# Kernel optimization log

Measured on AMD Instinct MI355X. Metric: run time of the kernel, lower is better.

Reference implementation:

```python
import jax, jax.numpy as jnp
import numpy as np

B, S, D = 32, 2048, 1024


def setup_inputs() -> dict:
    key = jax.random.key(0)
    k = jax.random.split(key, 7)
    midi_features = jax.random.normal(k[0], (B, S, D), dtype=jnp.float32)
    scale_id = jax.random.randint(k[1], (B,), 0, 3)
    midi_mask = jax.random.randint(k[2], (B, S), 0, 2).astype(jnp.int32)
    # Stacked branch params: index 0=high, 1=mid, 2=low (matches SCALE_TO_ID)
    W = jax.random.normal(k[3], (3, D, D), dtype=jnp.float32) * 0.02  # Linear weight (out,in)
    b = jax.random.normal(k[4], (3, D), dtype=jnp.float32) * 0.02
    scale_embed = jax.random.normal(k[5], (3, D), dtype=jnp.float32) * 0.02
    branch_embed = jax.random.normal(k[6], (3, D), dtype=jnp.float32) * 0.02
    return {"midi_features": midi_features, "scale_id": scale_id, "midi_mask": midi_mask,
            "W": W, "b": b, "scale_embed": scale_embed, "branch_embed": branch_embed}


def reference(midi_features, scale_id, midi_mask, W, b, scale_embed, branch_embed):
    # Per-sample scale routing: gather the branch's Linear weight for each sample
    # (equivalent to the torch fancy-indexing scatter into out[idx]).
    Wb = W[scale_id]               # (B, D, D) torch Linear convention: y = x @ W.T + b
    bb = b[scale_id]               # (B, D)
    out = jax.nn.silu(jnp.einsum('bsd,bed->bse', midi_features, Wb) + bb[:, None, :])
    # Dropout is identity in eval mode.
    out = out + scale_embed[scale_id][:, None, :]       # (B, S, D)

    seq_mask = midi_mask > 0                             # (B, S) bool
    w = seq_mask.astype(out.dtype)[:, :, None]           # (B, S, 1)
    denom = jnp.maximum(w.sum(axis=1), 1e-6)             # (B, 1)
    low_vec = (out * w).sum(axis=1) / denom              # (B, D) masked mean

    high_cond = out + branch_embed[0]                    # (B, S, D)
    mid_cond = out + branch_embed[1]                     # (B, S, D)
    low_cond = low_vec[:, None, :] + branch_embed[2]     # (B, 1, D) weak_low_alignment=True
    return high_cond, mid_cond, low_cond
```

## Files before the change

kernel.cpp:

```cpp
#include <hip/hip_runtime.h>
#include <hip/hip_bf16.h>

#define B_ 32
#define S_ 2048
#define D_ 1024

#define BM 256
#define BN 256
#define BK 64
#define NKT (D_ / BK)

typedef __attribute__((ext_vector_type(8))) short bf16x8;
typedef __attribute__((ext_vector_type(4))) float f32x4;
typedef __attribute__((ext_vector_type(4))) float float4v;

#define AS1 __attribute__((address_space(1)))
#define AS3 __attribute__((address_space(3)))

__device__ __forceinline__ short f2bf(float f) {
    union { float f; unsigned u; } uf;
    uf.f = f;
    unsigned u = uf.u;
    u += 0x7FFFu + ((u >> 16) & 1u);
    return (short)(u >> 16);
}

__global__ __launch_bounds__(256) void cvt_bf16(const float4v* __restrict__ src,
                                                bf16x8* __restrict__ dst, int n8) {
    const int stride = gridDim.x * blockDim.x;
    for (int i = blockIdx.x * blockDim.x + threadIdx.x; i < n8; i += stride) {
        float4v a = src[2 * i], b = src[2 * i + 1];
        bf16x8 v;
#pragma unroll
        for (int j = 0; j < 4; ++j) {
            v[j]     = f2bf(a[j]);
            v[4 + j] = f2bf(b[j]);
        }
        dst[i] = v;
    }
}


#define STAGE_A(nb, h, kt) do {                                               \
    _Pragma("unroll")                                                         \
    for (int j_ = 0; j_ < 2; ++j_) {                                          \
        const int base_ = (h) * 128 + j_ * 64 + wid * 8;                      \
        const int grow_ = j_ * 128 + (h) * 64 + wid * 8 + lrow8;              \
        const __hip_bfloat16* g_ = aBase + (size_t)grow_ * D_ + (kt) * BK + (scb >> 1); \
        __builtin_amdgcn_global_load_lds((const AS1 unsigned int*)g_,         \
            (AS3 unsigned int*)&As[nb][base_ * 64], 16, 0, 0);                \
    } } while (0)

#define STAGE_B(nb, h, kt) do {                                               \
    _Pragma("unroll")                                                         \
    for (int j_ = 0; j_ < 2; ++j_) {                                          \
        const int base_ = (h) * 128 + j_ * 64 + wid * 8;                      \
        const int grow_ = base_ + lrow8;                                      \
        const __hip_bfloat16* g_ = bBase + (size_t)grow_ * D_ + (kt) * BK + (scb >> 1); \
        __builtin_amdgcn_global_load_lds((const AS1 unsigned int*)g_,         \
            (AS3 unsigned int*)&Bs[nb][base_ * 64], 16, 0, 0);                \
    } } while (0)

#define COMPUTE(cur, mh, bh) do {                                             \
    bf16x8 af_[4][2], bv_[2][2];                                              \
    _Pragma("unroll")                                                         \
    for (int mi_ = 0; mi_ < 4; ++mi_) {                                       \
        const int l_ = (mh) * 128 + wm * 64 + mi_ * 16 + fr;                  \
        _Pragma("unroll")                                                     \
        for (int kk_ = 0; kk_ < 2; ++kk_) {                                   \
            const int byt_ = l_ * 128 + ((kk_ * 64 + fg * 16) ^ ((l_ & 7) << 4)); \
            af_[mi_][kk_] = *(const bf16x8*)((const char*)&As[cur][0] + byt_); \
        }                                                                     \
    }                                                                         \
    _Pragma("unroll")                                                         \
    for (int ni_ = 0; ni_ < 2; ++ni_) {                                       \
        const int l_ = (bh) * 128 + wn * 32 + ni_ * 16 + fr;                  \
        _Pragma("unroll")                                                     \
        for (int kk_ = 0; kk_ < 2; ++kk_) {                                   \
            const int byt_ = l_ * 128 + ((kk_ * 64 + fg * 16) ^ ((l_ & 7) << 4)); \
            bv_[ni_][kk_] = *(const bf16x8*)((const char*)&Bs[cur][0] + byt_); \
        }                                                                     \
    }                                                                         \
    __builtin_amdgcn_s_setprio(1);                                            \
    _Pragma("unroll")                                                         \
    for (int mi_ = 0; mi_ < 4; ++mi_)                                         \
        _Pragma("unroll")                                                     \
        for (int ni_ = 0; ni_ < 2; ++ni_)                                     \
            _Pragma("unroll")                                                 \
            for (int kk_ = 0; kk_ < 2; ++kk_)                                 \
                acc[(mh) * 4 + mi_][(bh) * 2 + ni_] =                         \
                    __builtin_amdgcn_mfma_f32_16x16x32_bf16(                  \
                        af_[mi_][kk_], bv_[ni_][kk_],                         \
                        acc[(mh) * 4 + mi_][(bh) * 2 + ni_], 0, 0, 0);        \
    __builtin_amdgcn_s_setprio(0);                                            \
    } while (0)

#define PWAIT() do {                                      \
    asm volatile("s_waitcnt vmcnt(6)" ::: "memory");      \
    asm volatile("s_barrier" ::: "memory"); } while (0)

__global__ __launch_bounds__(512, 2) void fused_gemm_bf16(
    const __hip_bfloat16* __restrict__ aBf,
    const __hip_bfloat16* __restrict__ wBf,
    const int*   __restrict__ scale_id,
    const int*   __restrict__ mask,
    const float* __restrict__ bias,
    const float* __restrict__ scemb,
    const float* __restrict__ bremb,
    float*       __restrict__ out,
    float*       __restrict__ colws)
{
    __shared__ __align__(16) short As[2][BM * BK];
    __shared__ __align__(16) short Bs[2][BM * BK];

    const int tid = threadIdx.x;
    const int lane = tid & 63;
    const int wid = tid >> 6;
    const int wm = wid >> 2;
    const int wn = wid & 3;

    const int NTI = D_ / BN;
    const int MTI = S_ / BM;
    const int NWG = B_ * MTI * NTI;
    const int CPX = NWG / 8;
    int lid = ((int)blockIdx.x % 8) * CPX + ((int)blockIdx.x / 8);
    int nt = lid % NTI;
    int mt = (lid / NTI) % MTI;
    int bb = lid / (NTI * MTI);

    const int sid = scale_id[bb];
    const __hip_bfloat16* aBase = aBf + ((size_t)bb * S_ + (size_t)mt * BM) * D_;
    const __hip_bfloat16* bBase = wBf + ((size_t)sid * D_ + (size_t)nt * BN) * D_;

    const int lrow8 = lane >> 3;
    const int scb = ((lane & 7) * 16) ^ (lrow8 << 4);

    const int fr = lane & 15;
    const int fg = lane >> 4;

    f32x4 acc[8][4];
#pragma unroll
    for (int mi = 0; mi < 8; ++mi)
#pragma unroll
        for (int ni = 0; ni < 4; ++ni)
            acc[mi][ni] = (f32x4){0.f, 0.f, 0.f, 0.f};

    STAGE_B(0, 0, 0); STAGE_A(0, 0, 0); STAGE_B(0, 1, 0); STAGE_A(0, 1, 0);

    for (int kt = 0; kt < NKT; kt += 2) {
        const int k1 = kt + 1;
        const int k1n = (k1 + 1 < NKT) ? k1 + 1 : k1;
        STAGE_B(1, 0, k1);  PWAIT(); COMPUTE(0, 0, 0);
        STAGE_A(1, 0, k1);  PWAIT(); COMPUTE(0, 0, 1);
        STAGE_B(1, 1, k1);  PWAIT(); COMPUTE(0, 1, 0);
        STAGE_A(1, 1, k1);  PWAIT(); COMPUTE(0, 1, 1);
        STAGE_B(0, 0, k1n); PWAIT(); COMPUTE(1, 0, 0);
        STAGE_A(0, 0, k1n); PWAIT(); COMPUTE(1, 0, 1);
        STAGE_B(0, 1, k1n); PWAIT(); COMPUTE(1, 1, 0);
        STAGE_A(0, 1, k1n); PWAIT(); COMPUTE(1, 1, 1);
    }

    __syncthreads();

    const int colb = nt * BN;
    float bv2[2][2], sv2[2][2];
#pragma unroll
    for (int bh = 0; bh < 2; ++bh)
#pragma unroll
        for (int ni = 0; ni < 2; ++ni) {
            const int n = colb + bh * 128 + wn * 32 + ni * 16 + fr;
            bv2[bh][ni] = bias[sid * D_ + n];
            sv2[bh][ni] = scemb[sid * D_ + n];
        }

    float colsum[2][2] = {{0.f, 0.f}, {0.f, 0.f}};
#pragma unroll
    for (int mig = 0; mig < 8; ++mig) {
        const int mrow0 = mt * BM + wm * 128 + mig * 16 + fg * 4;
        float mk[4];
#pragma unroll
        for (int r = 0; r < 4; ++r)
            mk[r] = (mask[(size_t)bb * S_ + mrow0 + r] > 0) ? 1.f : 0.f;
#pragma unroll
        for (int bh = 0; bh < 2; ++bh)
#pragma unroll
            for (int ni = 0; ni < 2; ++ni)
#pragma unroll
                for (int r = 0; r < 4; ++r) {
                    const float v = acc[mig][bh * 2 + ni][r] + bv2[bh][ni];
                    const float o = v / (1.f + __expf(-v)) + sv2[bh][ni];
                    acc[mig][bh * 2 + ni][r] = o;
                    colsum[bh][ni] += mk[r] * o;
                }
    }

#pragma unroll
    for (int bh = 0; bh < 2; ++bh)
#pragma unroll
        for (int ni = 0; ni < 2; ++ni) {
            float s = colsum[bh][ni];
            s += __shfl_xor(s, 16);
            s += __shfl_xor(s, 32);
            if (fg == 0)
                atomicAdd(&colws[(size_t)bb * D_ + (colb + bh * 128 + wn * 32 + ni * 16 + fr)], s);
        }

    float* ldsF = (float*)&As[0][0];
    const float4v b0 = *(const float4v*)&bremb[0 * D_ + colb + lane * 4];
    const float4v b1 = *(const float4v*)&bremb[1 * D_ + colb + lane * 4];
    const size_t MIDOFF = (size_t)B_ * S_ * D_;

#pragma unroll
    for (int mig = 0; mig < 8; ++mig) {
#pragma unroll
        for (int bh = 0; bh < 2; ++bh)
#pragma unroll
            for (int ni = 0; ni < 2; ++ni)
#pragma unroll
                for (int r = 0; r < 4; ++r)
                    ldsF[(wm * 16 + fg * 4 + r) * 260 + bh * 128 + wn * 32 + ni * 16 + fr] =
                        acc[mig][bh * 2 + ni][r];
        __syncthreads();

#pragma unroll
        for (int k = 0; k < 4; ++k) {
            const int lr = wid * 4 + k;
            const int grow = mt * BM + (lr >> 4) * 128 + mig * 16 + (lr & 15);
            const size_t rowbase = ((size_t)bb * S_ + grow) * D_ + colb;
            float4v v = *(const float4v*)&ldsF[lr * 260 + lane * 4];
            __builtin_nontemporal_store(v + b0, (float4v*)&out[rowbase + lane * 4]);
            __builtin_nontemporal_store(v + b1, (float4v*)&out[MIDOFF + rowbase + lane * 4]);
        }
        __syncthreads();
    }
}

#define FBM 128
#define FBN 128
#define FBK 64
#define FNK (D_ / FBK)

__global__ __launch_bounds__(256, 2) void fused_gemm_f32(
    const float* __restrict__ midi,
    const int*   __restrict__ scale_id,
    const int*   __restrict__ mask,
    const float* __restrict__ W,
    const float* __restrict__ bias,
    const float* __restrict__ scemb,
    const float* __restrict__ bremb,
    float*       __restrict__ out,
    float*       __restrict__ ws)
{
    __shared__ __align__(16) short As[FBM * FBK];
    __shared__ __align__(16) short Bs[FBM * FBK];

    const int tid = threadIdx.x;
    const int NTI = D_ / FBN;
    const int MTI = S_ / FBM;
    const int NWG = B_ * MTI * NTI;
    const int CPX = NWG / 8;
    int lid = ((int)blockIdx.x % 8) * CPX + ((int)blockIdx.x / 8);
    int nt = lid % NTI;
    int mt = (lid / NTI) % MTI;
    int bb = lid / (NTI * MTI);

    const int sid = scale_id[bb];
    const float* aBase = midi + ((size_t)bb * S_ + (size_t)mt * FBM) * D_;
    const float* bBase = W + ((size_t)sid * D_ + (size_t)nt * FBN) * D_;

    const int r0 = tid >> 3;
    const int kp = (tid & 7) * 8;

    float4v aL[4], aH[4], bL[4], bH[4];

    auto load_regs = [&](int kt) {
        const int kc = kt * FBK + kp;
#pragma unroll
        for (int i = 0; i < 4; ++i) {
            const float* pa = aBase + (size_t)(r0 + 32 * i) * D_ + kc;
            aL[i] = *(const float4v*)pa;
            aH[i] = *(const float4v*)(pa + 4);
            const float* pb = bBase + (size_t)(r0 + 32 * i) * D_ + kc;
            bL[i] = *(const float4v*)pb;
            bH[i] = *(const float4v*)(pb + 4);
        }
    };

    auto write_lds = [&]() {
#pragma unroll
        for (int i = 0; i < 4; ++i) {
            const int row = r0 + 32 * i;
            const int off = (row * FBK + kp) ^ ((row & 7) << 3);
            bf16x8 va, vb;
#pragma unroll
            for (int j = 0; j < 4; ++j) {
                va[j]     = f2bf(aL[i][j]);
                va[4 + j] = f2bf(aH[i][j]);
                vb[j]     = f2bf(bL[i][j]);
                vb[4 + j] = f2bf(bH[i][j]);
            }
            *(bf16x8*)&As[off] = va;
            *(bf16x8*)&Bs[off] = vb;
        }
    };

    f32x4 acc[4][4];
#pragma unroll
    for (int mi = 0; mi < 4; ++mi)
#pragma unroll
        for (int ni = 0; ni < 4; ++ni)
            acc[mi][ni] = (f32x4){0.f, 0.f, 0.f, 0.f};

    const int lane = tid & 63;
    const int wid = tid >> 6;
    const int wm = wid >> 1, wn = wid & 1;
    const int fr = lane & 15;
    const int fg = lane >> 4;

    load_regs(0);
    write_lds();
    __syncthreads();

    for (int kt = 0; kt < FNK; ++kt) {
        if (kt + 1 < FNK) load_regs(kt + 1);
#pragma unroll
        for (int kk = 0; kk < 2; ++kk) {
            bf16x8 af[4], bfr[4];
#pragma unroll
            for (int mi = 0; mi < 4; ++mi) {
                const int row = wm * 64 + mi * 16 + fr;
                const int off = (row * FBK + kk * 32 + fg * 8) ^ ((row & 7) << 3);
                af[mi] = *(const bf16x8*)&As[off];
            }
#pragma unroll
            for (int ni = 0; ni < 4; ++ni) {
                const int row = wn * 64 + ni * 16 + fr;
                const int off = (row * FBK + kk * 32 + fg * 8) ^ ((row & 7) << 3);
                bfr[ni] = *(const bf16x8*)&Bs[off];
            }
#pragma unroll
            for (int mi = 0; mi < 4; ++mi)
#pragma unroll
                for (int ni = 0; ni < 4; ++ni)
                    acc[mi][ni] = __builtin_amdgcn_mfma_f32_16x16x32_bf16(
                        af[mi], bfr[ni], acc[mi][ni], 0, 0, 0);
        }
        __syncthreads();
        if (kt + 1 < FNK) write_lds();
        __syncthreads();
    }

    const int ncolbase = nt * FBN + wn * 64;
    float bv[4], sv[4], b0v[4], b1v[4];
#pragma unroll
    for (int ni = 0; ni < 4; ++ni) {
        const int n = ncolbase + ni * 16 + fr;
        bv[ni]  = bias[sid * D_ + n];
        sv[ni]  = scemb[sid * D_ + n];
        b0v[ni] = bremb[0 * D_ + n];
        b1v[ni] = bremb[1 * D_ + n];
    }

    const size_t MIDOFF = (size_t)B_ * S_ * D_;
    float colsum[4] = {0.f, 0.f, 0.f, 0.f};

#pragma unroll
    for (int mi = 0; mi < 4; ++mi) {
        const int mrow0 = mt * FBM + wm * 64 + mi * 16 + fg * 4;
        float mk[4];
#pragma unroll
        for (int r = 0; r < 4; ++r)
            mk[r] = (mask[(size_t)bb * S_ + mrow0 + r] > 0) ? 1.f : 0.f;
#pragma unroll
        for (int ni = 0; ni < 4; ++ni) {
            const int n = ncolbase + ni * 16 + fr;
#pragma unroll
            for (int r = 0; r < 4; ++r) {
                const float v = acc[mi][ni][r] + bv[ni];
                const float o = v / (1.f + __expf(-v)) + sv[ni];
                const size_t idx = ((size_t)bb * S_ + (size_t)(mrow0 + r)) * D_ + n;
                __builtin_nontemporal_store(o + b0v[ni], &out[idx]);
                __builtin_nontemporal_store(o + b1v[ni], &out[MIDOFF + idx]);
                colsum[ni] += mk[r] * o;
            }
        }
    }

#pragma unroll
    for (int ni = 0; ni < 4; ++ni) {
        float s = colsum[ni];
        s += __shfl_xor(s, 16);
        s += __shfl_xor(s, 32);
        if (fg == 0)
            atomicAdd(&ws[(size_t)bb * D_ + (ncolbase + ni * 16 + fr)], s);
    }
}

__global__ void finalize(const int* __restrict__ mask,
                         const float* __restrict__ ws,
                         const float* __restrict__ bremb,
                         float* __restrict__ out)
{
    const int b = blockIdx.x;
    const int tid = threadIdx.x;

    int c = 0;
    for (int s = tid; s < S_; s += 256)
        c += (mask[(size_t)b * S_ + s] > 0) ? 1 : 0;
#pragma unroll
    for (int m = 1; m < 64; m <<= 1)
        c += __shfl_xor(c, m);

    __shared__ int part[4];
    if ((tid & 63) == 0) part[tid >> 6] = c;
    __syncthreads();
    const float denom = fmaxf((float)(part[0] + part[1] + part[2] + part[3]), 1e-6f);
    const float inv = 1.f / denom;

    const size_t LOWOFF = (size_t)2 * B_ * S_ * D_;
    for (int e = tid; e < D_; e += 256)
        out[LOWOFF + (size_t)b * D_ + e] = ws[(size_t)b * D_ + e] * inv + bremb[2 * D_ + e];
}

extern "C" void kernel_launch(void* const* d_in, const int* in_sizes, int n_in,
                              void* d_out, int out_size, void* d_ws, size_t ws_size,
                              hipStream_t stream) {
    const float* midi     = (const float*)d_in[0];
    const int*   scale_id = (const int*)d_in[1];
    const int*   mask     = (const int*)d_in[2];
    const float* W        = (const float*)d_in[3];
    const float* bias     = (const float*)d_in[4];
    const float* scemb    = (const float*)d_in[5];
    const float* bremb    = (const float*)d_in[6];
    float* out = (float*)d_out;
    float* colws = (float*)d_ws;

    const size_t COLWS_B = (size_t)B_ * D_ * sizeof(float);
    const size_t WBF_B   = (size_t)3 * D_ * D_ * sizeof(short);
    const size_t ABF_B   = (size_t)B_ * S_ * D_ * sizeof(short);
    const size_t need    = COLWS_B + WBF_B + ABF_B;

    hipMemsetAsync(colws, 0, COLWS_B, stream);

    if (ws_size >= need) {
        __hip_bfloat16* wBf = (__hip_bfloat16*)((char*)d_ws + COLWS_B);
        __hip_bfloat16* aBf = (__hip_bfloat16*)((char*)d_ws + COLWS_B + WBF_B);
        cvt_bf16<<<dim3(2048), dim3(256), 0, stream>>>(
            (const float4v*)midi, (bf16x8*)aBf, (B_ * S_ * D_) / 8);
        cvt_bf16<<<dim3(512), dim3(256), 0, stream>>>(
            (const float4v*)W, (bf16x8*)wBf, (3 * D_ * D_) / 8);
        fused_gemm_bf16<<<dim3(B_ * (S_ / BM) * (D_ / BN)), dim3(512), 0, stream>>>(
            aBf, wBf, scale_id, mask, bias, scemb, bremb, out, colws);
    } else {
        fused_gemm_f32<<<dim3(B_ * (S_ / FBM) * (D_ / FBN)), dim3(256), 0, stream>>>(
            midi, scale_id, mask, W, bias, scemb, bremb, out, colws);
    }

    finalize<<<dim3(B_), dim3(256), 0, stream>>>(mask, colws, bremb, out);
}
```

Measured before the change: 317.9 us.

## Restructure bf16 GEMM pipeline to one barrier per K-tile with full prefetch

Replaces the fine-grained interleaving of eight stage/wait/compute quarter-steps per K-tile pair with a simpler double-buffer schedule. Each iteration issues all loads for the next tile, runs all four compute quarters on the current tile, then waits for all memory ops (vmcnt(0)) and does a single barrier. The aim is fewer barriers and waitcnt stalls. The trade-off is less fine-grained overlap and a full drain of outstanding loads at each tile boundary. The f32 kernel's shared arrays are also renamed, which has no speed effect.

Result: faster. 309.0 us (-2.8%).

```diff
diff --git a/kernel.cpp b/kernel.cpp
--- a/kernel.cpp
+++ b/kernel.cpp
@@ -95,9 +95,19 @@
     __builtin_amdgcn_s_setprio(0);                                            \
     } while (0)
 
-#define PWAIT() do {                                      \
-    asm volatile("s_waitcnt vmcnt(6)" ::: "memory");      \
+#define BOUND() do {                                          \
+    asm volatile("s_waitcnt vmcnt(0)" ::: "memory");          \
     asm volatile("s_barrier" ::: "memory"); } while (0)
+
+#define BODY(X, Y, kn) do {                                                   \
+    STAGE_B(Y, 0, kn); STAGE_A(Y, 0, kn); STAGE_B(Y, 1, kn); STAGE_A(Y, 1, kn); \
+    COMPUTE(X, 0, 0); COMPUTE(X, 0, 1); COMPUTE(X, 1, 0); COMPUTE(X, 1, 1);   \
+    BOUND();                                                                  \
+} while (0)
+
+#define BODY_LAST(X) do {                                                     \
+    COMPUTE(X, 0, 0); COMPUTE(X, 0, 1); COMPUTE(X, 1, 0); COMPUTE(X, 1, 1);   \
+} while (0)
 
 __global__ __launch_bounds__(512, 2) void fused_gemm_bf16(
     const __hip_bfloat16* __restrict__ aBf,
@@ -146,19 +156,15 @@
             acc[mi][ni] = (f32x4){0.f, 0.f, 0.f, 0.f};
 
     STAGE_B(0, 0, 0); STAGE_A(0, 0, 0); STAGE_B(0, 1, 0); STAGE_A(0, 1, 0);
-
-    for (int kt = 0; kt < NKT; kt += 2) {
-        const int k1 = kt + 1;
-        const int k1n = (k1 + 1 < NKT) ? k1 + 1 : k1;
-        STAGE_B(1, 0, k1);  PWAIT(); COMPUTE(0, 0, 0);
-        STAGE_A(1, 0, k1);  PWAIT(); COMPUTE(0, 0, 1);
-        STAGE_B(1, 1, k1);  PWAIT(); COMPUTE(0, 1, 0);
-        STAGE_A(1, 1, k1);  PWAIT(); COMPUTE(0, 1, 1);
-        STAGE_B(0, 0, k1n); PWAIT(); COMPUTE(1, 0, 0);
-        STAGE_A(0, 0, k1n); PWAIT(); COMPUTE(1, 0, 1);
-        STAGE_B(0, 1, k1n); PWAIT(); COMPUTE(1, 1, 0);
-        STAGE_A(0, 1, k1n); PWAIT(); COMPUTE(1, 1, 1);
-    }
+    BOUND();
+
+#pragma unroll 1
+    for (int kt = 0; kt < NKT - 2; kt += 2) {
+        BODY(0, 1, kt + 1);
+        BODY(1, 0, kt + 2);
+    }
+    BODY(0, 1, NKT - 1);
+    BODY_LAST(1);
 
     __syncthreads();
 
@@ -251,8 +257,8 @@
     float*       __restrict__ out,
     float*       __restrict__ ws)
 {
-    __shared__ __align__(16) short As[FBM * FBK];
-    __shared__ __align__(16) short Bs[FBM * FBK];
+    __shared__ __align__(16) short Asf[FBM * FBK];
+    __shared__ __align__(16) short Bsf[FBM * FBK];
 
     const int tid = threadIdx.x;
     const int NTI = D_ / FBN;
@@ -299,8 +305,8 @@
                 vb[j]     = f2bf(bL[i][j]);
                 vb[4 + j] = f2bf(bH[i][j]);
             }
-            *(bf16x8*)&As[off] = va;
-            *(bf16x8*)&Bs[off] = vb;
+            *(bf16x8*)&Asf[off] = va;
+            *(bf16x8*)&Bsf[off] = vb;
         }
     };
 
@@ -330,13 +336,13 @@
             for (int mi = 0; mi < 4; ++mi) {
                 const int row = wm * 64 + mi * 16 + fr;
                 const int off = (row * FBK + kk * 32 + fg * 8) ^ ((row & 7) << 3);
-                af[mi] = *(const bf16x8*)&As[off];
+                af[mi] = *(const bf16x8*)&Asf[off];
             }
 #pragma unroll
             for (int ni = 0; ni < 4; ++ni) {
                 const int row = wn * 64 + ni * 16 + fr;
                 const int off = (row * FBK + kk * 32 + fg * 8) ^ ((row & 7) << 3);
-                bfr[ni] = *(const bf16x8*)&Bs[off];
+                bfr[ni] = *(const bf16x8*)&Bsf[off];
             }
 #pragma unroll
             for (int mi = 0; mi < 4; ++mi)
```
